# Optimization experiments

Hardware: AMD Instinct MI355X
Metric: run time of the kernel (lower is better)

Reference implementation:

```python
import jax, jax.numpy as jnp
import numpy as np

STRIDE = 4

_LENGTHS = np.array([131070, 131074, 131069, 131075, 131072, 131071, 131073, 131072], dtype=np.int64)
assert _LENGTHS.sum() == 1048576


def setup_inputs() -> dict:
    key = jax.random.key(0)
    k1, k2, k3, k4 = jax.random.split(key, 4)
    N = int(_LENGTHS.sum())
    C_in, C_out = 96, 192
    feat = jax.random.normal(k1, (N, C_in), dtype=jnp.float32)
    coord = jax.random.normal(k2, (N, 3), dtype=jnp.float32)
    scores = jax.random.uniform(k3, (N,), dtype=jnp.float32)
    W = jax.random.normal(k4, (C_in, C_out), dtype=jnp.float32) * (1.0 / np.sqrt(C_in))
    b = jnp.zeros((C_out,), dtype=jnp.float32)
    lengths = jnp.asarray(_LENGTHS)
    batch = jnp.asarray(np.repeat(np.arange(len(_LENGTHS), dtype=np.int64), _LENGTHS))
    return {"feat": feat, "coord": coord, "scores": scores, "W": W, "b": b,
            "lengths": lengths, "batch": batch}


def _window_segments(lengths_np, batch):
    # per-point window-segment id for ragged windowed pooling
    offsets = np.concatenate([[0], np.cumsum(lengths_np)])          # [B+1]
    n_win = -(-lengths_np // STRIDE)                                 # ceil(L/stride), [B]
    win_off = np.concatenate([[0], np.cumsum(n_win)])                # [B+1]
    N = int(offsets[-1])
    M = int(win_off[-1])
    pos = jnp.arange(N) - jnp.asarray(offsets)[batch]                # position within batch
    seg = jnp.asarray(win_off)[batch] + pos // STRIDE                # [N] segment id
    return seg, M, n_win


def reference(feat, coord, scores, W, b, lengths, batch):
    lengths_np = np.asarray(lengths)
    seg, M, n_win = _window_segments(lengths_np, batch)
    counts = jax.ops.segment_sum(jnp.ones(feat.shape[0], feat.dtype), seg, num_segments=M)
    inv = 1.0 / counts
    # mean pooling per window (segment reduce), single pass over the data
    feat_down = jax.ops.segment_sum(feat, seg, num_segments=M) * inv[:, None]
    coord_down = jax.ops.segment_sum(coord, seg, num_segments=M) * inv[:, None]
    scores_down = jax.ops.segment_sum(scores, seg, num_segments=M) * inv
    batch_down = jnp.asarray(np.repeat(np.arange(len(lengths_np), dtype=np.int64), n_win))
    # proj + (Identity norm) + ReLU
    feat_out = jax.nn.relu(feat_down @ W + b)
    lengths_down = jnp.asarray(n_win)
    offset_down = jnp.cumsum(lengths_down)
    return feat_out, coord_down, batch_down, scores_down, lengths_down, offset_down
```

## Files before the change

### kernel.cpp

```cpp
#include <hip/hip_runtime.h>

#define CIN 96
#define COUT 192
#define SW 4
#define BM 128
#define KPA 96
#define KPW 104

typedef __attribute__((ext_vector_type(8))) short bf16x8;
typedef __attribute__((ext_vector_type(4))) float f32x4;

__device__ __forceinline__ short f2bf(float x) {
  unsigned int u;
  __builtin_memcpy(&u, &x, 4);
  u += 0x7fffu + ((u >> 16) & 1u);
  return (short)(u >> 16);
}

__global__ __launch_bounds__(256) void fused_kernel(
    const float* __restrict__ feat, const float* __restrict__ coord,
    const float* __restrict__ scores, const float* __restrict__ W,
    const float* __restrict__ bias, const int* __restrict__ lengths, int B,
    float* __restrict__ out) {
  __shared__ short A_lds[BM * KPA];
  __shared__ short Wt_lds[COUT * KPW];
  __shared__ int s_meta[BM];

  const int tid = threadIdx.x;
  const long long m0 = (long long)blockIdx.x * BM;

  long long M = 0;
  for (int i = 0; i < B; ++i) M += ((long long)lengths[i] + (SW - 1)) >> 2;

  long long startL = 0; int cntL = 0, bfL = 0;
  if (tid < BM) {
    long long m = m0 + tid;
    long long off = 0, woff = 0;
    for (int i = 0; i < B; ++i) {
      long long L = lengths[i];
      long long nw = (L + (SW - 1)) >> 2;
      if (m >= woff && m < woff + nw) {
        long long st = off + (m - woff) * SW;
        long long rem = off + L - st;
        startL = st;
        cntL = (int)(rem < (long long)SW ? rem : (long long)SW);
        bfL = i;
      }
      off += L; woff += nw;
    }
    s_meta[tid] = (int)startL | (cntL << 28);
  }
  __syncthreads();

  #pragma unroll 4
  for (int i = 0; i < 12; ++i) {
    int task = tid + 256 * i;
    int w = task / 24;
    int g = task - w * 24;
    int mv = s_meta[w];
    int cw = (int)((unsigned)mv >> 28);
    int st = mv & 0x0FFFFFFF;
    const float* fp = feat + (long long)st * CIN + g * 4;
    float sx = 0.f, sy = 0.f, sz = 0.f, sw2 = 0.f;
    for (int p = 0; p < cw; ++p) {
      float4 v = *(const float4*)(fp + p * CIN);
      sx += v.x; sy += v.y; sz += v.z; sw2 += v.w;
    }
    float inv = cw ? 1.0f / (float)cw : 0.f;
    short4 h;
    h.x = f2bf(sx * inv); h.y = f2bf(sy * inv);
    h.z = f2bf(sz * inv); h.w = f2bf(sw2 * inv);
    *(short4*)&A_lds[w * KPA + g * 4] = h;
  }

  #pragma unroll 3
  for (int i = 0; i < 9; ++i) {
    int task = tid + 256 * i;
    int kg = task / COUT;
    int n = task - kg * COUT;
    const float* wp = W + kg * 8 * COUT + n;
    bf16x8 hv;
    #pragma unroll
    for (int j = 0; j < 8; ++j) hv[j] = f2bf(wp[j * COUT]);
    *(bf16x8*)&Wt_lds[n * KPW + kg * 8] = hv;
  }

  if (tid < BM) {
    long long m = m0 + tid;
    if (m < M) {
      float cx = 0.f, cy = 0.f, cz = 0.f, ss = 0.f;
      const float* cp = coord + startL * 3;
      for (int p = 0; p < cntL; ++p) {
        cx += cp[p * 3 + 0]; cy += cp[p * 3 + 1]; cz += cp[p * 3 + 2];
        ss += scores[startL + p];
      }
      float inv = 1.0f / (float)cntL;
      long long o1 = M * (long long)COUT;
      long long o2 = o1 + M * 3;
      long long o3 = o2 + M;
      out[o1 + m * 3 + 0] = cx * inv;
      out[o1 + m * 3 + 1] = cy * inv;
      out[o1 + m * 3 + 2] = cz * inv;
      out[o2 + m] = (float)bfL;
      out[o3 + m] = ss * inv;
    }
  }
  if (blockIdx.x == 0 && tid == 0) {
    long long o4 = M * (long long)(COUT + 3 + 1 + 1);
    long long cum = 0;
    for (int i = 0; i < B; ++i) {
      long long nw = ((long long)lengths[i] + (SW - 1)) >> 2;
      out[o4 + i] = (float)nw;
      cum += nw;
      out[o4 + B + i] = (float)cum;
    }
  }

  __syncthreads();

  const int wv = tid >> 6;
  const int lane = tid & 63;
  const int lm = lane & 15;
  const int quad = lane >> 4;

  bf16x8 af[2][3];
  #pragma unroll
  for (int mt = 0; mt < 2; ++mt)
    #pragma unroll
    for (int ks = 0; ks < 3; ++ks)
      af[mt][ks] = *(const bf16x8*)&A_lds[(wv * 32 + mt * 16 + lm) * KPA + ks * 32 + quad * 8];

  f32x4 acc[2][12];
  #pragma unroll
  for (int mt = 0; mt < 2; ++mt)
    #pragma unroll
    for (int nt = 0; nt < 12; ++nt)
      acc[mt][nt] = (f32x4){0.f, 0.f, 0.f, 0.f};

  #pragma unroll
  for (int nt = 0; nt < 12; ++nt) {
    const int nrow = nt * 16 + lm;
    #pragma unroll
    for (int ks = 0; ks < 3; ++ks) {
      bf16x8 bfr = *(const bf16x8*)&Wt_lds[nrow * KPW + ks * 32 + quad * 8];
      acc[0][nt] = __builtin_amdgcn_mfma_f32_16x16x32_bf16(af[0][ks], bfr, acc[0][nt], 0, 0, 0);
      acc[1][nt] = __builtin_amdgcn_mfma_f32_16x16x32_bf16(af[1][ks], bfr, acc[1][nt], 0, 0, 0);
    }
  }

  #pragma unroll
  for (int nt = 0; nt < 12; ++nt) {
    int col = nt * 16 + lm;
    float bv = bias[col];
    #pragma unroll
    for (int mt = 0; mt < 2; ++mt) {
      long long rbase = m0 + wv * 32 + mt * 16 + quad * 4;
      #pragma unroll
      for (int r = 0; r < 4; ++r) {
        long long m = rbase + r;
        if (m < M) {
          float x = acc[mt][nt][r] + bv;
          out[m * COUT + col] = x > 0.f ? x : 0.f;
        }
      }
    }
  }
}

extern "C" void kernel_launch(void* const* d_in, const int* in_sizes, int n_in,
                              void* d_out, int out_size, void* d_ws, size_t ws_size,
                              hipStream_t stream) {
  const float* feat    = (const float*)d_in[0];
  const float* coord   = (const float*)d_in[1];
  const float* scores  = (const float*)d_in[2];
  const float* W       = (const float*)d_in[3];
  const float* bias    = (const float*)d_in[4];
  const int*   lengths = (const int*)d_in[5];
  float* out = (float*)d_out;

  const int N = in_sizes[2];
  const int B = in_sizes[5];
  const int Mmax = N / SW + B;

  const int blocks = (Mmax + BM - 1) / BM;
  fused_kernel<<<blocks, 256, 0, stream>>>(feat, coord, scores, W, bias, lengths, B, out);
}
```

Baseline: 680.7 us.

## Split fused pool+GEMM into separate pooling and MFMA GEMM kernels via workspace

Replaces the single fused kernel with two kernels. The first pools windows with one thread per window and channel group, loads all four rows unconditionally with masks, writes bf16 pooled features and a bf16 transposed W to workspace, and also emits coord, score and batch outputs. The second kernel stages W into LDS and runs the MFMA GEMM with 512 threads, each wave covering 16 rows. This removes the per-block W conversion and the serial pooling work that stalled the fused kernel, at the cost of an extra write and read of the pooled matrix through global memory and a second launch.

```diff
diff --git a/kernel.cpp b/kernel.cpp
--- a/kernel.cpp
+++ b/kernel.cpp
@@ -6,6 +6,9 @@
 #define BM 128
 #define KPA 96
 #define KPW 104
+#define TPB_A 256
+#define TPT_A 8
+#define TPB_B 512
 
 typedef __attribute__((ext_vector_type(8))) short bf16x8;
 typedef __attribute__((ext_vector_type(4))) float f32x4;
@@ -15,6 +18,173 @@
   __builtin_memcpy(&u, &x, 4);
   u += 0x7fffu + ((u >> 16) & 1u);
   return (short)(u >> 16);
+}
+
+__global__ __launch_bounds__(TPB_A) void pool_kernel(
+    const float* __restrict__ feat, const float* __restrict__ coord,
+    const float* __restrict__ scores, const float* __restrict__ W,
+    const int* __restrict__ lengths, int B,
+    short* __restrict__ wsA, short* __restrict__ wsWt,
+    float* __restrict__ out) {
+  int M = 0;
+  for (int i = 0; i < B; ++i) M += (lengths[i] + (SW - 1)) >> 2;
+  const int R0 = M * 24;
+  const int R1 = R0 + M;
+  const int R2 = R1 + COUT * 12;
+
+  const int base = blockIdx.x * (TPB_A * TPT_A) + threadIdx.x;
+
+  #pragma unroll
+  for (int u = 0; u < TPT_A; ++u) {
+    const int t = base + u * TPB_A;
+    if (t < R0) {
+      const int w = t / 24;
+      const int g = t - w * 24;
+      int off = 0, woff = 0, st = 0, cw = 0;
+      for (int i = 0; i < B; ++i) {
+        const int L = lengths[i];
+        const int nw = (L + (SW - 1)) >> 2;
+        if (w >= woff && w < woff + nw) {
+          st = off + (w - woff) * SW;
+          const int rem = off + L - st;
+          cw = rem < SW ? rem : SW;
+        }
+        off += L; woff += nw;
+      }
+      const float* fp = feat + (long long)st * CIN + g * 4;
+      float4 v0 = *(const float4*)(fp);
+      float4 v1 = *(const float4*)(fp + CIN);
+      float4 v2 = *(const float4*)(fp + 2 * CIN);
+      float4 v3 = *(const float4*)(fp + 3 * CIN);
+      const float k1 = (cw > 1) ? 1.f : 0.f;
+      const float k2 = (cw > 2) ? 1.f : 0.f;
+      const float k3 = (cw > 3) ? 1.f : 0.f;
+      float sx = v0.x + k1 * v1.x + k2 * v2.x + k3 * v3.x;
+      float sy = v0.y + k1 * v1.y + k2 * v2.y + k3 * v3.y;
+      float sz = v0.z + k1 * v1.z + k2 * v2.z + k3 * v3.z;
+      float sw2 = v0.w + k1 * v1.w + k2 * v2.w + k3 * v3.w;
+      const float inv = 1.0f / (float)cw;
+      short4 h;
+      h.x = f2bf(sx * inv); h.y = f2bf(sy * inv);
+      h.z = f2bf(sz * inv); h.w = f2bf(sw2 * inv);
+      *(short4*)&wsA[(long long)w * CIN + g * 4] = h;
+    } else if (t < R1) {
+      const int m = t - R0;
+      int off = 0, woff = 0, st = 0, cw = 0, bf = 0;
+      for (int i = 0; i < B; ++i) {
+        const int L = lengths[i];
+        const int nw = (L + (SW - 1)) >> 2;
+        if (m >= woff && m < woff + nw) {
+          st = off + (m - woff) * SW;
+          const int rem = off + L - st;
+          cw = rem < SW ? rem : SW;
+          bf = i;
+        }
+        off += L; woff += nw;
+      }
+      const float* cp = coord + (long long)st * 3;
+      const float* sp = scores + st;
+      float cx = 0.f, cy = 0.f, cz = 0.f, ss = 0.f;
+      #pragma unroll
+      for (int p = 0; p < 4; ++p) {
+        const float mk = (p < cw) ? 1.f : 0.f;
+        cx = fmaf(mk, cp[p * 3 + 0], cx);
+        cy = fmaf(mk, cp[p * 3 + 1], cy);
+        cz = fmaf(mk, cp[p * 3 + 2], cz);
+        ss = fmaf(mk, sp[p], ss);
+      }
+      const float inv = 1.0f / (float)cw;
+      const long long o1 = (long long)M * COUT;
+      const long long o2 = o1 + (long long)M * 3;
+      const long long o3 = o2 + M;
+      out[o1 + (long long)m * 3 + 0] = cx * inv;
+      out[o1 + (long long)m * 3 + 1] = cy * inv;
+      out[o1 + (long long)m * 3 + 2] = cz * inv;
+      out[o2 + m] = (float)bf;
+      out[o3 + m] = ss * inv;
+    } else if (t < R2) {
+      const int j = t - R1;
+      const int kg = j / COUT;
+      const int n = j - kg * COUT;
+      const float* wp = W + (long long)kg * 8 * COUT + n;
+      bf16x8 hv;
+      #pragma unroll
+      for (int q = 0; q < 8; ++q) hv[q] = f2bf(wp[q * COUT]);
+      *(bf16x8*)&wsWt[n * KPW + kg * 8] = hv;
+    }
+  }
+
+  if (blockIdx.x == 0 && threadIdx.x == 0) {
+    const long long o4 = (long long)M * (COUT + 3 + 1 + 1);
+    long long cum = 0;
+    for (int i = 0; i < B; ++i) {
+      const long long nw = ((long long)lengths[i] + (SW - 1)) >> 2;
+      out[o4 + i] = (float)nw;
+      cum += nw;
+      out[o4 + B + i] = (float)cum;
+    }
+  }
+}
+
+__global__ __launch_bounds__(TPB_B) void gemm_kernel(
+    const short* __restrict__ wsA, const short* __restrict__ wsWt,
+    const float* __restrict__ bias, const int* __restrict__ lengths, int B,
+    float* __restrict__ out) {
+  __shared__ alignas(16) short Wt_lds[COUT * KPW];
+
+  int M = 0;
+  for (int i = 0; i < B; ++i) M += (lengths[i] + (SW - 1)) >> 2;
+
+  const int tid = threadIdx.x;
+  const long long m0 = (long long)blockIdx.x * BM;
+  const int wv = tid >> 6;
+  const int lane = tid & 63;
+  const int lm = lane & 15;
+  const int quad = lane >> 4;
+
+  bf16x8 af[3];
+  const short* arow = wsA + (m0 + wv * 16 + lm) * CIN;
+  #pragma unroll
+  for (int ks = 0; ks < 3; ++ks)
+    af[ks] = *(const bf16x8*)(arow + ks * 32 + quad * 8);
+
+  const float4* src = (const float4*)wsWt;
+  float4* dst = (float4*)Wt_lds;
+  #pragma unroll
+  for (int i = 0; i < 5; ++i) {
+    const int idx = tid + TPB_B * i;
+    if (idx < (COUT * KPW * 2 / 16)) dst[idx] = src[idx];
+  }
+  __syncthreads();
+
+  f32x4 acc[12];
+  #pragma unroll
+  for (int nt = 0; nt < 12; ++nt) acc[nt] = (f32x4){0.f, 0.f, 0.f, 0.f};
+
+  #pragma unroll
+  for (int nt = 0; nt < 12; ++nt) {
+    const int nrow = nt * 16 + lm;
+    #pragma unroll
+    for (int ks = 0; ks < 3; ++ks) {
+      bf16x8 bfr = *(const bf16x8*)&Wt_lds[nrow * KPW + ks * 32 + quad * 8];
+      acc[nt] = __builtin_amdgcn_mfma_f32_16x16x32_bf16(af[ks], bfr, acc[nt], 0, 0, 0);
+    }
+  }
+
+  #pragma unroll
+  for (int nt = 0; nt < 12; ++nt) {
+    const int col = nt * 16 + lm;
+    const float bv = bias[col];
+    const long long rbase = m0 + wv * 16 + quad * 4;
+    #pragma unroll
+    for (int r = 0; r < 4; ++r) {
+      const long long m = rbase + r;
+      if (m < M) {
+        const float x = acc[nt][r] + bv;
+        out[m * COUT + col] = x > 0.f ? x : 0.f;
+      }
+    }
+  }
 }
 
 __global__ __launch_bounds__(256) void fused_kernel(
@@ -182,6 +352,22 @@
   const int B = in_sizes[5];
   const int Mmax = N / SW + B;
 
-  const int blocks = (Mmax + BM - 1) / BM;
-  fused_kernel<<<blocks, 256, 0, stream>>>(feat, coord, scores, W, bias, lengths, B, out);
-}
+  const int blocksB = (Mmax + BM - 1) / BM;
+  const long long Mpad = (long long)blocksB * BM;
+  const size_t A_bytes = (size_t)Mpad * CIN * sizeof(short);
+  const size_t WT_bytes = (size_t)COUT * KPW * sizeof(short);
+
+  if (ws_size >= A_bytes + WT_bytes) {
+    short* wsA = (short*)d_ws;
+    short* wsWt = (short*)((char*)d_ws + A_bytes);
+    const long long Tmax = (long long)Mmax * 25 + COUT * 12;
+    const int blocksA = (int)((Tmax + (long long)TPB_A * TPT_A - 1) /
+                              ((long long)TPB_A * TPT_A));
+    pool_kernel<<<blocksA, TPB_A, 0, stream>>>(feat, coord, scores, W, lengths,
+                                               B, wsA, wsWt, out);
+    gemm_kernel<<<blocksB, TPB_B, 0, stream>>>(wsA, wsWt, bias, lengths, B, out);
+  } else {
+    fused_kernel<<<blocksB, 256, 0, stream>>>(feat, coord, scores, W, bias,
+                                              lengths, B, out);
+  }
+}
```

After: 651.8 us. -4.2%, faster.
